# Optimization experiments

Hardware: AMD Instinct MI355X
Metric: run time of the kernel (lower is better)

The kernel has to match this reference:

```python
import jax, jax.numpy as jnp
import numpy as np

EMBEDDING_DIM = 1024

def _pe_table(seq_len, dim, dtype):
    pos = jnp.arange(seq_len, dtype=jnp.float32)[:, None]        # [S,1]
    i = jnp.arange(dim)                                          # [D]
    k = (i // 2).astype(jnp.float32)                             # i//2 per source
    # NOTE: source uses exponent k/dim (not 2k/dim) -- faithful to the code
    angle = pos / jnp.power(10000.0, k / dim)                    # [S,D]
    pe = jnp.where((i % 2) == 0, jnp.sin(angle), jnp.cos(angle))
    return pe.astype(dtype)


def setup_inputs() -> dict:
    key = jax.random.key(0)
    x = jax.random.normal(key, (8, 4096, EMBEDDING_DIM), dtype=jnp.float32)
    return {"x": x}


def reference(x) -> jnp.ndarray:
    B, S, D = x.shape
    pe = _pe_table(S, D, x.dtype)          # [S,D]
    return x + pe[None, :, :]              # broadcast over batch
```

## Files before the change

kernel.cpp:

```cpp
#include <hip/hip_runtime.h>


#define PE_B 8
#define PE_S 4096
#define PE_D 1024

typedef float v4f __attribute__((ext_vector_type(4)));

__global__ __launch_bounds__(256) void pe_add_kernel(
    const float* __restrict__ x, float* __restrict__ out) {
    const int tid = blockIdx.x * blockDim.x + threadIdx.x;
    const int i   = (tid & (PE_D / 4 - 1)) * 4;
    const int s   = tid >> 8;

    const size_t off    = (size_t)tid * 4;
    const size_t stride = (size_t)PE_S * PE_D;

    v4f v[PE_B];
#pragma unroll
    for (int b = 0; b < PE_B; ++b)
        v[b] = *(const v4f*)(x + b * stride + off);

    const float pos = (float)s;
    const float c   = -13.287712379549449f / (float)PE_D;
    const float k0  = (float)(i >> 1);
    const float a0  = pos * exp2f(k0 * c);
    const float a1  = pos * exp2f((k0 + 1.0f) * c);
    float s0, c0, s1, c1;
    sincosf(a0, &s0, &c0);
    sincosf(a1, &s1, &c1);
    const v4f pe = {s0, c0, s1, c1};

#pragma unroll
    for (int b = 0; b < PE_B; ++b) {
        const v4f r = v[b] + pe;
        __builtin_nontemporal_store(r, (v4f*)(out + b * stride + off));
    }
}

extern "C" void kernel_launch(void* const* d_in, const int* in_sizes, int n_in,
                              void* d_out, int out_size, void* d_ws, size_t ws_size,
                              hipStream_t stream) {
    const float* x = (const float*)d_in[0];
    float* out = (float*)d_out;
    const int threads = PE_S * PE_D / 4;
    pe_add_kernel<<<threads / 256, 256, 0, stream>>>(x, out);
}
```

Baseline: 251.8 us.

## Precompute positional-encoding table in workspace and stream one vector per thread

```diff
diff --git a/kernel.cpp b/kernel.cpp
--- a/kernel.cpp
+++ b/kernel.cpp
@@ -4,22 +4,14 @@
 #define PE_B 8
 #define PE_S 4096
 #define PE_D 1024
+#define ROW4 (PE_S * PE_D / 4)
 
 typedef float v4f __attribute__((ext_vector_type(4)));
 
-__global__ __launch_bounds__(256) void pe_add_kernel(
-    const float* __restrict__ x, float* __restrict__ out) {
+__global__ __launch_bounds__(256) void pe_table_kernel(v4f* __restrict__ pe_tab) {
     const int tid = blockIdx.x * blockDim.x + threadIdx.x;
     const int i   = (tid & (PE_D / 4 - 1)) * 4;
     const int s   = tid >> 8;
-
-    const size_t off    = (size_t)tid * 4;
-    const size_t stride = (size_t)PE_S * PE_D;
-
-    v4f v[PE_B];
-#pragma unroll
-    for (int b = 0; b < PE_B; ++b)
-        v[b] = *(const v4f*)(x + b * stride + off);
 
     const float pos = (float)s;
     const float c   = -13.287712379549449f / (float)PE_D;
@@ -30,12 +22,37 @@
     sincosf(a0, &s0, &c0);
     sincosf(a1, &s1, &c1);
     const v4f pe = {s0, c0, s1, c1};
+    pe_tab[tid] = pe;
+}
 
-#pragma unroll
-    for (int b = 0; b < PE_B; ++b) {
-        const v4f r = v[b] + pe;
-        __builtin_nontemporal_store(r, (v4f*)(out + b * stride + off));
-    }
+__global__ __launch_bounds__(256) void pe_add_kernel(
+    const float* __restrict__ x, const v4f* __restrict__ pe_tab,
+    float* __restrict__ out) {
+    const int idx = blockIdx.x * blockDim.x + threadIdx.x;
+    const v4f v = *(const v4f*)(x + (size_t)idx * 4);
+    const v4f p = pe_tab[idx & (ROW4 - 1)];
+    *(v4f*)(out + (size_t)idx * 4) = v + p;
+}
+
+__global__ __launch_bounds__(256) void pe_fused_kernel(
+    const float* __restrict__ x, float* __restrict__ out) {
+    const int idx = blockIdx.x * blockDim.x + threadIdx.x;
+    const int r   = idx & (ROW4 - 1);
+    const int i   = (r & (PE_D / 4 - 1)) * 4;
+    const int s   = r >> 8;
+
+    const v4f v = *(const v4f*)(x + (size_t)idx * 4);
+
+    const float pos = (float)s;
+    const float c   = -13.287712379549449f / (float)PE_D;
+    const float k0  = (float)(i >> 1);
+    const float a0  = pos * exp2f(k0 * c);
+    const float a1  = pos * exp2f((k0 + 1.0f) * c);
+    float s0, c0, s1, c1;
+    sincosf(a0, &s0, &c0);
+    sincosf(a1, &s1, &c1);
+    const v4f pe = {s0, c0, s1, c1};
+    *(v4f*)(out + (size_t)idx * 4) = v + pe;
 }
 
 extern "C" void kernel_launch(void* const* d_in, const int* in_sizes, int n_in,
@@ -43,6 +60,13 @@
                               hipStream_t stream) {
     const float* x = (const float*)d_in[0];
     float* out = (float*)d_out;
-    const int threads = PE_S * PE_D / 4;
-    pe_add_kernel<<<threads / 256, 256, 0, stream>>>(x, out);
+    const int n4 = PE_B * ROW4;
+
+    if (ws_size >= (size_t)PE_S * PE_D * sizeof(float)) {
+        v4f* pe_tab = (v4f*)d_ws;
+        pe_table_kernel<<<ROW4 / 256, 256, 0, stream>>>(pe_tab);
+        pe_add_kernel<<<n4 / 256, 256, 0, stream>>>(x, pe_tab, out);
+    } else {
+        pe_fused_kernel<<<n4 / 256, 256, 0, stream>>>(x, out);
+    }
 }
```

Measured after the change: 228.2 us. 1.1x faster.
